# Performance work log

Measured on AMD Instinct MI355X. Metric: run time of the kernel, lower is better.

The kernel has to match this reference:

```python
import jax, jax.numpy as jnp
import numpy as np

N_HEADS = 16
E = 1024
HEAD = E // N_HEADS

def setup_inputs() -> dict:
    key = jax.random.key(0)
    k1, k2, k3, k4 = jax.random.split(key, 4)
    x = jax.random.normal(k1, (4, 2048, E), dtype=jnp.float32)
    # Linear weights stored as (in, out) for x @ W
    W_kqv = jax.random.normal(k2, (E, 3 * E), dtype=jnp.float32) * (E ** -0.5)
    W_proj = jax.random.normal(k3, (E, E), dtype=jnp.float32) * (E ** -0.5)
    b_proj = jax.random.normal(k4, (E,), dtype=jnp.float32) * 0.02
    return {"x": x, "W_kqv": W_kqv, "W_proj": W_proj, "b_proj": b_proj}

def reference(x, W_kqv, W_proj, b_proj):
    B, T, Edim = x.shape
    kqv = x @ W_kqv  # [B,T,3E]
    k, q, v = jnp.split(kqv, 3, axis=-1)
    # [B,T,E] -> [B,H,T,D]
    def to_heads(t):
        return t.reshape(B, T, N_HEADS, HEAD).transpose(0, 2, 1, 3)
    k, q, v = to_heads(k), to_heads(q), to_heads(v)
    att = jnp.einsum('bhqd,bhkd->bhqk', q, k) * (HEAD ** -0.5)
    causal = jnp.tril(jnp.ones((T, T), dtype=bool))
    att = jnp.where(causal[None, None], att, jnp.float32(-jnp.inf))
    att = jax.nn.softmax(att, axis=-1)  # dropout p=0 (eval)
    x_att = jnp.einsum('bhqk,bhkd->bhqd', att, v)
    x_att = x_att.transpose(0, 2, 1, 3).reshape(B, T, Edim)
    return x_att @ W_proj + b_proj
```

## Files before the change

### kernel.cpp

```cpp
#include <hip/hip_runtime.h>
#include <hip/hip_bf16.h>


typedef __bf16 bf16_t;
typedef __bf16 bf16x8 __attribute__((ext_vector_type(8)));
typedef __bf16 bf16x4 __attribute__((ext_vector_type(4)));
typedef float  f32x4  __attribute__((ext_vector_type(4)));

#define GLD16(gp, lp) __builtin_amdgcn_global_load_lds(                        \
    (const __attribute__((address_space(1))) void*)(gp),                       \
    (__attribute__((address_space(3))) void*)(lp), 16, 0, 0)

static constexpr int kB = 4, kT = 2048, kE = 1024, kH = 16, kD = 64;
static constexpr int kM = kB * kT;
static constexpr int kN1 = 3 * kE;
static constexpr float kScale = 0.125f;
static constexpr float kShift = 10.0f;

__global__ void cvt_f32_bf16(const float* __restrict__ in,
                             bf16_t* __restrict__ out, int n4) {
  int i = blockIdx.x * 256 + threadIdx.x;
  if (i >= n4) return;
  float4 f = reinterpret_cast<const float4*>(in)[i];
  bf16x4 o = { (bf16_t)f.x, (bf16_t)f.y, (bf16_t)f.z, (bf16_t)f.w };
  reinterpret_cast<bf16x4*>(out)[i] = o;
}

__global__ void transpose_tile(const float* __restrict__ W,
                               bf16_t* __restrict__ Wt, int K, int N) {
  __shared__ bf16_t t[64][65];
  const int k0 = blockIdx.x * 64, n0 = blockIdx.y * 64;
  const int c = threadIdx.x & 63, r4 = threadIdx.x >> 6;
#pragma unroll
  for (int i = 0; i < 16; i++) {
    const int kk = r4 * 16 + i;
    t[kk][c] = (bf16_t)W[(size_t)(k0 + kk) * N + n0 + c];
  }
  __syncthreads();
#pragma unroll
  for (int i = 0; i < 16; i++) {
    const int nn = r4 * 16 + i;
    Wt[(size_t)(n0 + nn) * K + k0 + c] = t[c][nn];
  }
}

template <int MODE>
__global__ __launch_bounds__(256, 2)
void gemm_bt(const bf16_t* __restrict__ A, const bf16_t* __restrict__ Bt,
             float* __restrict__ Cout, const float* __restrict__ bias,
             bf16_t* __restrict__ Kh, bf16_t* __restrict__ Qh,
             bf16_t* __restrict__ Vt, int M, int N, int K) {
  constexpr int BM = 128, BN = 128, BK = 64;
  __shared__ __align__(16) bf16_t As[BM * BK];
  __shared__ __align__(16) bf16_t Bs[BN * BK];
  const int tid = threadIdx.x;
  const int lane = tid & 63, wave = tid >> 6;
  const int m0 = blockIdx.y * BM, n0 = blockIdx.x * BN;
  const int wr = (wave >> 1) * 64, wc = (wave & 1) * 64;
  const int l15 = lane & 15, l4 = lane >> 4;
  const int r8 = lane >> 3, c8 = lane & 7;

  f32x4 acc[4][4];
#pragma unroll
  for (int m = 0; m < 4; m++)
#pragma unroll
    for (int n = 0; n < 4; n++) acc[m][n] = f32x4{0.f, 0.f, 0.f, 0.f};

  for (int k0 = 0; k0 < K; k0 += BK) {
    const bf16_t* Ag = A + (size_t)(m0 + wave * 32) * K + k0;
    const bf16_t* Bg = Bt + (size_t)(n0 + wave * 32) * K + k0;
    bf16_t* Al = As + wave * 32 * BK;
    bf16_t* Bl = Bs + wave * 32 * BK;
#pragma unroll
    for (int i = 0; i < 4; i++) {
      GLD16(Ag + (size_t)(i * 8 + r8) * K + c8 * 8, Al + i * 8 * BK);
      GLD16(Bg + (size_t)(i * 8 + r8) * K + c8 * 8, Bl + i * 8 * BK);
    }
    __syncthreads();
#pragma unroll
    for (int ks = 0; ks < 2; ks++) {
      bf16x8 af[4], bfr[4];
#pragma unroll
      for (int m = 0; m < 4; m++)
        af[m] = *reinterpret_cast<const bf16x8*>(
            As + (wr + m * 16 + l15) * BK + ks * 32 + l4 * 8);
#pragma unroll
      for (int n = 0; n < 4; n++)
        bfr[n] = *reinterpret_cast<const bf16x8*>(
            Bs + (wc + n * 16 + l15) * BK + ks * 32 + l4 * 8);
#pragma unroll
      for (int m = 0; m < 4; m++)
#pragma unroll
        for (int n = 0; n < 4; n++)
          acc[m][n] = __builtin_amdgcn_mfma_f32_16x16x32_bf16(
              af[m], bfr[n], acc[m][n], 0, 0, 0);
    }
    __syncthreads();
  }

#pragma unroll
  for (int m = 0; m < 4; m++) {
#pragma unroll
    for (int n = 0; n < 4; n++) {
      const int gcol = n0 + wc + n * 16 + l15;
      const int growb = m0 + wr + m * 16 + l4 * 4;
      if constexpr (MODE == 0) {
        const int seg = gcol >> 10, idx = gcol & 1023;
        const int h = idx >> 6, d = idx & 63;
        const int b = growb >> 11, t = growb & 2047;
        if (seg == 2) {
          bf16x4 pv = { (bf16_t)acc[m][n][0], (bf16_t)acc[m][n][1],
                        (bf16_t)acc[m][n][2], (bf16_t)acc[m][n][3] };
          *reinterpret_cast<bf16x4*>(
              Vt + ((size_t)(b * 16 + h) * 64 + d) * 2048 + t) = pv;
        } else {
          bf16_t* tgt = (seg == 0) ? Kh : Qh;
          const float sc = (seg == 1) ? kScale : 1.0f;
#pragma unroll
          for (int j = 0; j < 4; j++)
            tgt[((size_t)(b * 16 + h) * 2048 + (t + j)) * 64 + d] =
                (bf16_t)(acc[m][n][j] * sc);
        }
      } else {
        const float bv = bias[gcol];
#pragma unroll
        for (int j = 0; j < 4; j++)
          Cout[(size_t)(growb + j) * N + gcol] = acc[m][n][j] + bv;
      }
    }
  }
}

__global__ __launch_bounds__(256, 3)
void attn_fwd(const bf16_t* __restrict__ Qh, const bf16_t* __restrict__ Kh,
              const bf16_t* __restrict__ Vt, bf16_t* __restrict__ xatt) {
  const int bx = blockIdx.x;
  const int qt = 15 - (bx >> 6);
  const int bh = bx & 63;
  const int b = bh >> 4, h = bh & 15;
  const bf16_t* Qp = Qh + (size_t)bh * kT * kD;
  const bf16_t* Kp = Kh + (size_t)bh * kT * kD;
  const bf16_t* Vp = Vt + (size_t)bh * kD * kT;
  __shared__ __align__(16) bf16_t Ks[2][64 * 64];
  __shared__ __align__(16) bf16_t Vs[2][64 * 64];
  __shared__ __align__(16) bf16_t Ps[128 * 64];
  const int tid = threadIdx.x, lane = tid & 63, wave = tid >> 6;
  const int l15 = lane & 15, l4 = lane >> 4;
  const int r8 = lane >> 3, c8 = lane & 7;
  const int qr = wave * 32;
  const int swc = (c8 ^ r8) * 8;
  const int swr = (l15 & 7) * 8;
  const int q0 = qt * 128;
  const int nkt = qt * 2 + 2;

  auto stage = [&](int buf, int kt) {
    const int k0 = kt * 64;
#pragma unroll
    for (int i = 0; i < 2; i++) {
      const int row = wave * 16 + i * 8 + r8;
      GLD16(Kp + (size_t)(k0 + row) * kD + swc,
            Ks[buf] + (wave * 16 + i * 8) * 64);
      GLD16(Vp + (size_t)row * kT + k0 + swc,
            Vs[buf] + (wave * 16 + i * 8) * 64);
    }
  };

  bf16x8 qf[2][2];
#pragma unroll
  for (int m = 0; m < 2; m++)
#pragma unroll
    for (int ks = 0; ks < 2; ks++)
      qf[m][ks] = *reinterpret_cast<const bf16x8*>(
          Qp + (size_t)(q0 + qr + m * 16 + l15) * kD + ks * 32 + l4 * 8);

  bf16x8 ones;
#pragma unroll
  for (int e = 0; e < 8; e++) ones[e] = (bf16_t)1.0f;

  f32x4 oacc[2][4];
  f32x4 lacc[2];
#pragma unroll
  for (int m = 0; m < 2; m++) {
    lacc[m] = f32x4{0.f, 0.f, 0.f, 0.f};
#pragma unroll
    for (int dn = 0; dn < 4; dn++) oacc[m][dn] = f32x4{0.f, 0.f, 0.f, 0.f};
  }

  stage(0, 0);
  __syncthreads();
  int cur = 0;
  for (int kt = 0; kt < nkt; kt++) {
    const int k0 = kt * 64;
    if (kt + 1 < nkt) stage(cur ^ 1, kt + 1);

    const bool active = (k0 <= q0 + qr + 31);
    if (active) {
      f32x4 s[2][4];
#pragma unroll
      for (int m = 0; m < 2; m++)
#pragma unroll
        for (int n = 0; n < 4; n++) s[m][n] = f32x4{0.f, 0.f, 0.f, 0.f};
      __builtin_amdgcn_s_setprio(1);
#pragma unroll
      for (int ks = 0; ks < 2; ks++) {
        bf16x8 kf[4];
#pragma unroll
        for (int n = 0; n < 4; n++)
          kf[n] = *reinterpret_cast<const bf16x8*>(
              Ks[cur] + (n * 16 + l15) * 64 + (((ks * 4 + l4) * 8) ^ swr));
#pragma unroll
        for (int m = 0; m < 2; m++)
#pragma unroll
          for (int n = 0; n < 4; n++)
            s[m][n] = __builtin_amdgcn_mfma_f32_16x16x32_bf16(
                qf[m][ks], kf[n], s[m][n], 0, 0, 0);
      }
      __builtin_amdgcn_s_setprio(0);

      if (k0 + 63 > q0 + qr) {
#pragma unroll
        for (int m = 0; m < 2; m++)
#pragma unroll
          for (int n = 0; n < 4; n++)
#pragma unroll
            for (int j = 0; j < 4; j++) {
              const int qg = q0 + qr + m * 16 + l4 * 4 + j;
              const int kg = k0 + n * 16 + l15;
              if (kg > qg) s[m][n][j] = -__builtin_inff();
            }
      }

#pragma unroll
      for (int m = 0; m < 2; m++)
#pragma unroll
        for (int n = 0; n < 4; n++)
#pragma unroll
          for (int j = 0; j < 4; j++) {
            const int pr = qr + m * 16 + l4 * 4 + j;
            Ps[pr * 64 + ((n * 16 + l15) ^ ((pr & 7) << 3))] =
                (bf16_t)__expf(s[m][n][j] - kShift);
          }

      __builtin_amdgcn_s_setprio(1);
#pragma unroll
      for (int ks = 0; ks < 2; ks++) {
        bf16x8 pf[2], vf[4];
#pragma unroll
        for (int m = 0; m < 2; m++)
          pf[m] = *reinterpret_cast<const bf16x8*>(
              Ps + (qr + m * 16 + l15) * 64 + (((ks * 4 + l4) * 8) ^ swr));
#pragma unroll
        for (int dn = 0; dn < 4; dn++)
          vf[dn] = *reinterpret_cast<const bf16x8*>(
              Vs[cur] + (dn * 16 + l15) * 64 + (((ks * 4 + l4) * 8) ^ swr));
#pragma unroll
        for (int m = 0; m < 2; m++) {
#pragma unroll
          for (int dn = 0; dn < 4; dn++)
            oacc[m][dn] = __builtin_amdgcn_mfma_f32_16x16x32_bf16(
                pf[m], vf[dn], oacc[m][dn], 0, 0, 0);
          lacc[m] = __builtin_amdgcn_mfma_f32_16x16x32_bf16(
              pf[m], ones, lacc[m], 0, 0, 0);
        }
      }
      __builtin_amdgcn_s_setprio(0);
    }
    __syncthreads();
    cur ^= 1;
  }

#pragma unroll
  for (int m = 0; m < 2; m++) {
    float inv[4];
#pragma unroll
    for (int j = 0; j < 4; j++) inv[j] = 1.f / lacc[m][j];
#pragma unroll
    for (int dn = 0; dn < 4; dn++)
#pragma unroll
      for (int j = 0; j < 4; j++) {
        const int t = q0 + qr + m * 16 + l4 * 4 + j;
        const int col = h * 64 + dn * 16 + l15;
        xatt[((size_t)b * kT + t) * kE + col] =
            (bf16_t)(oacc[m][dn][j] * inv[j]);
      }
  }
}

extern "C" void kernel_launch(void* const* d_in, const int* in_sizes, int n_in,
                              void* d_out, int out_size, void* d_ws,
                              size_t ws_size, hipStream_t stream) {
  const float* x     = (const float*)d_in[0];
  const float* Wkqv  = (const float*)d_in[1];
  const float* Wproj = (const float*)d_in[2];
  const float* bproj = (const float*)d_in[3];
  float* out = (float*)d_out;

  char* ws = (char*)d_ws;
  bf16_t* xb     = (bf16_t*)(ws);
  bf16_t* WkqvT  = (bf16_t*)(ws + 16777216);
  bf16_t* WprojT = (bf16_t*)(ws + 23068672);
  bf16_t* Qh     = (bf16_t*)(ws + 25165824);
  bf16_t* Kh     = (bf16_t*)(ws + 41943040);
  bf16_t* Vt     = (bf16_t*)(ws + 58720256);
  bf16_t* xatt   = (bf16_t*)(ws + 75497472);

  cvt_f32_bf16<<<(kM * kE / 4 + 255) / 256, 256, 0, stream>>>(x, xb, kM * kE / 4);
  transpose_tile<<<dim3(kE / 64, kN1 / 64), 256, 0, stream>>>(Wkqv, WkqvT, kE, kN1);
  transpose_tile<<<dim3(kE / 64, kE / 64), 256, 0, stream>>>(Wproj, WprojT, kE, kE);

  gemm_bt<0><<<dim3(kN1 / 128, kM / 128), 256, 0, stream>>>(
      xb, WkqvT, nullptr, nullptr, Kh, Qh, Vt, kM, kN1, kE);

  attn_fwd<<<dim3(16 * 64), 256, 0, stream>>>(Qh, Kh, Vt, xatt);

  gemm_bt<1><<<dim3(kE / 128, kM / 128), 256, 0, stream>>>(
      xatt, WprojT, out, bproj, nullptr, nullptr, nullptr, kM, kE, kE);
}
```

Measured before the change: 171.3 us.

## Rewrite GEMMs as 256x256 double-buffered 8-wave kernels with swizzled LDS

Replaces the 128x128 single-buffer GEMM with a 256x256-tile, 512-thread kernel. It double-buffers LDS with global_load_lds, overlaps the next tile's loads with MFMA phases using explicit vmcnt waits and barriers, and XOR-swizzles the LDS layout to cut bank conflicts. Block ids are remapped for L2 locality, and MFMA sections run at raised wave priority. Larger tiles raise reuse but use 128KB of LDS and more registers per block, which lowers occupancy. The projection GEMM also ends up with only 128 blocks.

```diff
diff --git a/kernel.cpp b/kernel.cpp
--- a/kernel.cpp
+++ b/kernel.cpp
@@ -10,6 +10,9 @@
 #define GLD16(gp, lp) __builtin_amdgcn_global_load_lds(                        \
     (const __attribute__((address_space(1))) void*)(gp),                       \
     (__attribute__((address_space(3))) void*)(lp), 16, 0, 0)
+
+#define WAITV(n) asm volatile("s_waitcnt vmcnt(" #n ")" ::: "memory")
+#define SBAR()   asm volatile("s_barrier" ::: "memory")
 
 static constexpr int kB = 4, kT = 2048, kE = 1024, kH = 16, kD = 64;
 static constexpr int kM = kB * kT;
@@ -45,87 +48,116 @@
 }
 
 template <int MODE>
-__global__ __launch_bounds__(256, 2)
-void gemm_bt(const bf16_t* __restrict__ A, const bf16_t* __restrict__ Bt,
-             float* __restrict__ Cout, const float* __restrict__ bias,
-             bf16_t* __restrict__ Kh, bf16_t* __restrict__ Qh,
-             bf16_t* __restrict__ Vt, int M, int N, int K) {
-  constexpr int BM = 128, BN = 128, BK = 64;
-  __shared__ __align__(16) bf16_t As[BM * BK];
-  __shared__ __align__(16) bf16_t Bs[BN * BK];
-  const int tid = threadIdx.x;
-  const int lane = tid & 63, wave = tid >> 6;
-  const int m0 = blockIdx.y * BM, n0 = blockIdx.x * BN;
-  const int wr = (wave >> 1) * 64, wc = (wave & 1) * 64;
+__global__ __launch_bounds__(512, 2)
+void gemm8p(const bf16_t* __restrict__ A, const bf16_t* __restrict__ Bt,
+            float* __restrict__ Cout, const float* __restrict__ bias,
+            bf16_t* __restrict__ Kh, bf16_t* __restrict__ Qh,
+            bf16_t* __restrict__ Vt, int M, int N, int K, int nbx, int cpx) {
+  __shared__ __align__(16) bf16_t As_[2][256 * 64];
+  __shared__ __align__(16) bf16_t Bs_[2][256 * 64];
+  const int tid = threadIdx.x, lane = tid & 63, wave = tid >> 6;
   const int l15 = lane & 15, l4 = lane >> 4;
-  const int r8 = lane >> 3, c8 = lane & 7;
-
-  f32x4 acc[4][4];
-#pragma unroll
-  for (int m = 0; m < 4; m++)
-#pragma unroll
-    for (int n = 0; n < 4; n++) acc[m][n] = f32x4{0.f, 0.f, 0.f, 0.f};
-
-  for (int k0 = 0; k0 < K; k0 += BK) {
-    const bf16_t* Ag = A + (size_t)(m0 + wave * 32) * K + k0;
-    const bf16_t* Bg = Bt + (size_t)(n0 + wave * 32) * K + k0;
-    bf16_t* Al = As + wave * 32 * BK;
-    bf16_t* Bl = Bs + wave * 32 * BK;
-#pragma unroll
-    for (int i = 0; i < 4; i++) {
-      GLD16(Ag + (size_t)(i * 8 + r8) * K + c8 * 8, Al + i * 8 * BK);
-      GLD16(Bg + (size_t)(i * 8 + r8) * K + c8 * 8, Bl + i * 8 * BK);
-    }
-    __syncthreads();
-#pragma unroll
-    for (int ks = 0; ks < 2; ks++) {
-      bf16x8 af[4], bfr[4];
-#pragma unroll
-      for (int m = 0; m < 4; m++)
-        af[m] = *reinterpret_cast<const bf16x8*>(
-            As + (wr + m * 16 + l15) * BK + ks * 32 + l4 * 8);
-#pragma unroll
-      for (int n = 0; n < 4; n++)
-        bfr[n] = *reinterpret_cast<const bf16x8*>(
-            Bs + (wc + n * 16 + l15) * BK + ks * 32 + l4 * 8);
-#pragma unroll
-      for (int m = 0; m < 4; m++)
-#pragma unroll
-        for (int n = 0; n < 4; n++)
-          acc[m][n] = __builtin_amdgcn_mfma_f32_16x16x32_bf16(
-              af[m], bfr[n], acc[m][n], 0, 0, 0);
-    }
-    __syncthreads();
-  }
-
-#pragma unroll
-  for (int m = 0; m < 4; m++) {
-#pragma unroll
-    for (int n = 0; n < 4; n++) {
-      const int gcol = n0 + wc + n * 16 + l15;
-      const int growb = m0 + wr + m * 16 + l4 * 4;
+  const int wr = wave >> 2, wc = wave & 3;
+
+  const int id = blockIdx.x;
+  const int sw = (id & 7) * cpx + (id >> 3);
+  const int m0 = (sw / nbx) * 256, n0 = (sw % nbx) * 256;
+  const int NT = K >> 6;
+  const bf16_t* Ag = A + (size_t)m0 * K;
+  const bf16_t* Bg = Bt + (size_t)n0 * K;
+
+  const int a_row_lane = ((tid >> 8) << 7) + ((tid >> 3) & 31);
+  const int b_row_lane = ((tid >> 7) << 6) + ((tid >> 3) & 15);
+  const int s_csrc = ((tid & 7) ^ ((tid >> 3) & 7)) << 3;
+  const int a_base = ((wave >> 2) << 7) + ((wave & 3) << 3);
+  const int b_base = ((wave >> 1) << 6) + ((wave & 1) << 3);
+
+#define STAGE(nb, kt, p) do {                                                  \
+    const int _k0 = (kt) << 6;                                                 \
+    GLD16(Ag + (size_t)(a_row_lane + (p) * 32) * K + _k0 + s_csrc,             \
+          As_[nb] + (a_base + (p) * 32) * 64);                                 \
+    GLD16(Bg + (size_t)(b_row_lane + (p) * 16) * K + _k0 + s_csrc,             \
+          Bs_[nb] + (b_base + (p) * 16) * 64);                                 \
+  } while (0)
+
+#define RDA(bi, r, ks) (*(const bf16x8*)(As_[bi] +                             \
+    (wr * 128 + (r) * 16 + l15) * 64 + ((((ks) * 4 + l4) ^ (l15 & 7)) << 3)))
+#define RDB(bi, c, ks) (*(const bf16x8*)(Bs_[bi] +                             \
+    (wc * 64 + (c) * 16 + l15) * 64 + ((((ks) * 4 + l4) ^ (l15 & 7)) << 3)))
+
+  f32x4 acc[8][4];
+#pragma unroll
+  for (int r = 0; r < 8; r++)
+#pragma unroll
+    for (int c = 0; c < 4; c++) acc[r][c] = f32x4{0.f, 0.f, 0.f, 0.f};
+  bf16x8 afr[4][2], bfr[2][2];
+
+  STAGE(0, 0, 0); STAGE(0, 0, 1); STAGE(0, 0, 2); STAGE(0, 0, 3);
+  WAITV(4);
+  SBAR();
+
+#define PHASE(bi, t, p, rb, cb, doA) do {                                      \
+    if (doA) {                                                                 \
+      _Pragma("unroll") for (int r = 0; r < 4; r++)                            \
+      _Pragma("unroll") for (int ks = 0; ks < 2; ks++)                         \
+        afr[r][ks] = RDA(bi, (rb) + r, ks);                                    \
+    }                                                                          \
+    if ((t) + 1 < NT) { STAGE((bi) ^ 1, (t) + 1, p); WAITV(4); }               \
+    else if ((p) == 0) { WAITV(2); }                                           \
+    else if ((p) == 1) { WAITV(0); }                                           \
+    SBAR();                                                                    \
+    _Pragma("unroll") for (int c = 0; c < 2; c++)                              \
+    _Pragma("unroll") for (int ks = 0; ks < 2; ks++)                           \
+      bfr[c][ks] = RDB(bi, (cb) + c, ks);                                      \
+    __builtin_amdgcn_s_setprio(1);                                             \
+    _Pragma("unroll") for (int ks = 0; ks < 2; ks++)                           \
+    _Pragma("unroll") for (int r = 0; r < 4; r++)                              \
+    _Pragma("unroll") for (int c = 0; c < 2; c++)                              \
+      acc[(rb) + r][(cb) + c] = __builtin_amdgcn_mfma_f32_16x16x32_bf16(       \
+          afr[r][ks], bfr[c][ks], acc[(rb) + r][(cb) + c], 0, 0, 0);           \
+    __builtin_amdgcn_s_setprio(0);                                             \
+  } while (0)
+
+#pragma unroll 1
+  for (int t = 0; t < NT; t++) {
+    const int bi = t & 1;
+    PHASE(bi, t, 0, 0, 0, true);
+    PHASE(bi, t, 1, 0, 2, false);
+    PHASE(bi, t, 2, 4, 0, true);
+    PHASE(bi, t, 3, 4, 2, false);
+    SBAR();
+  }
+#undef PHASE
+#undef STAGE
+
+#pragma unroll
+  for (int r = 0; r < 8; r++) {
+#pragma unroll
+    for (int c = 0; c < 4; c++) {
+      const int gcol = n0 + wc * 64 + c * 16 + l15;
+      const int grow = m0 + wr * 128 + r * 16 + l4 * 4;
       if constexpr (MODE == 0) {
         const int seg = gcol >> 10, idx = gcol & 1023;
         const int h = idx >> 6, d = idx & 63;
-        const int b = growb >> 11, t = growb & 2047;
+        const int b = grow >> 11, tt = grow & 2047;
         if (seg == 2) {
-          bf16x4 pv = { (bf16_t)acc[m][n][0], (bf16_t)acc[m][n][1],
-                        (bf16_t)acc[m][n][2], (bf16_t)acc[m][n][3] };
+          bf16x4 pv = { (bf16_t)acc[r][c][0], (bf16_t)acc[r][c][1],
+                        (bf16_t)acc[r][c][2], (bf16_t)acc[r][c][3] };
           *reinterpret_cast<bf16x4*>(
-              Vt + ((size_t)(b * 16 + h) * 64 + d) * 2048 + t) = pv;
+              Vt + ((size_t)(b * 16 + h) * 64 + d) * 2048 + tt) = pv;
         } else {
           bf16_t* tgt = (seg == 0) ? Kh : Qh;
           const float sc = (seg == 1) ? kScale : 1.0f;
 #pragma unroll
           for (int j = 0; j < 4; j++)
-            tgt[((size_t)(b * 16 + h) * 2048 + (t + j)) * 64 + d] =
-                (bf16_t)(acc[m][n][j] * sc);
+            tgt[((size_t)(b * 16 + h) * 2048 + (tt + j)) * 64 + d] =
+                (bf16_t)(acc[r][c][j] * sc);
         }
       } else {
         const float bv = bias[gcol];
 #pragma unroll
         for (int j = 0; j < 4; j++)
-          Cout[(size_t)(growb + j) * N + gcol] = acc[m][n][j] + bv;
+          Cout[(size_t)(grow + j) * N + gcol] = acc[r][c][j] + bv;
       }
     }
   }
@@ -308,11 +340,12 @@
   transpose_tile<<<dim3(kE / 64, kN1 / 64), 256, 0, stream>>>(Wkqv, WkqvT, kE, kN1);
   transpose_tile<<<dim3(kE / 64, kE / 64), 256, 0, stream>>>(Wproj, WprojT, kE, kE);
 
-  gemm_bt<0><<<dim3(kN1 / 128, kM / 128), 256, 0, stream>>>(
-      xb, WkqvT, nullptr, nullptr, Kh, Qh, Vt, kM, kN1, kE);
+  gemm8p<0><<<dim3((kM / 256) * (kN1 / 256)), 512, 0, stream>>>(
+      xb, WkqvT, nullptr, nullptr, Kh, Qh, Vt, kM, kN1, kE, kN1 / 256, 48);
 
   attn_fwd<<<dim3(16 * 64), 256, 0, stream>>>(Qh, Kh, Vt, xatt);
 
-  gemm_bt<1><<<dim3(kE / 128, kM / 128), 256, 0, stream>>>(
-      xatt, WprojT, out, bproj, nullptr, nullptr, nullptr, kM, kE, kE);
-}
+  gemm8p<1><<<dim3((kM / 256) * (kE / 256)), 512, 0, stream>>>(
+      xatt, WprojT, out, bproj, nullptr, nullptr, nullptr, kM, kE, kE,
+      kE / 256, 16);
+}
```

After: 207.0 us. +20.9%, slower.
